# Optimization experiments

Measured on AMD Instinct MI355X. Metric: run time of the kernel, lower is better.

Reference implementation:

```python
import jax, jax.numpy as jnp
import numpy as np

ROPE_THETA = 10000.0


def rope(t, rot_dim):
    """lucidrains-style rotary embedding: rotate first rot_dim features,
    interleaved (x0,x1) pairing; remaining features pass through.
    t: [B, S, D] with rot_dim <= D."""
    S = t.shape[-2]
    half = rot_dim // 2
    inv_freq = 1.0 / (ROPE_THETA ** (jnp.arange(0, rot_dim, 2, dtype=jnp.float32) / rot_dim))  # [half]
    freqs = jnp.arange(S, dtype=jnp.float32)[:, None] * inv_freq[None, :]  # [S, half]
    freqs = jnp.repeat(freqs, 2, axis=-1)  # [S, rot_dim]
    cos, sin = jnp.cos(freqs), jnp.sin(freqs)
    t_rot, t_pass = t[..., :rot_dim], t[..., rot_dim:]
    x = t_rot.reshape(*t_rot.shape[:-1], half, 2)
    rh = jnp.stack([-x[..., 1], x[..., 0]], axis=-1).reshape(t_rot.shape)  # rotate_half (interleaved)
    t_rot = t_rot * cos + rh * sin
    return jnp.concatenate([t_rot, t_pass], axis=-1)


def feature_map(x):
    # L2 normalize along the feature dim (Hydra-attention canonical choice)
    norm = jnp.sqrt(jnp.sum(x * x, axis=-1, keepdims=True))
    return x / jnp.maximum(norm, 1e-12)


def setup_inputs() -> dict:
    key = jax.random.key(0)
    kx, kwi, kwo = jax.random.split(key, 3)
    B, S, D = 8, 4096, 2048
    scale = 0.02  # keep activations numerically tame
    return {
        "X": jax.random.normal(kx, (B, S, D), dtype=jnp.float32),
        "W_in": jax.random.normal(kwi, (3 * D, D), dtype=jnp.float32) * scale,
        "b_in": jnp.zeros((3 * D,), dtype=jnp.float32),
        "W_out": jax.random.normal(kwo, (D, D), dtype=jnp.float32) * scale,
        "b_out": jnp.zeros((D,), dtype=jnp.float32),
    }


def reference(X, W_in, b_in, W_out, b_out):
    D = X.shape[-1]
    QKV = jnp.einsum("bsd,ed->bse", X, W_in) + b_in  # [B, S, 3D]
    Q, K, V = jnp.split(QKV, 3, axis=-1)
    rot_dim = D // 2  # RotaryEmbedding(feature_dim // 2)
    Q = rope(Q, rot_dim)
    K = rope(K, rot_dim)
    A = jnp.sum(feature_map(K) * V, axis=-2)  # [B, D] global sum over sequence
    Y = A[:, None, :] * Q  # [B, S, D]
    Y = jnp.einsum("bsd,ed->bse", Y, W_out) + b_out
    return Y + X
```

## Files before the change

### kernel.cpp

```cpp
#include <hip/hip_runtime.h>

#define N_TOK   32768L
#define DMODEL  2048L
#define E1      6144L
#define ROT     1024
#define SMASK   4095

typedef __attribute__((ext_vector_type(8))) _Float16 half8;
typedef __attribute__((ext_vector_type(4))) _Float16 half4;
typedef __attribute__((ext_vector_type(4))) float    floatx4;
typedef __attribute__((ext_vector_type(4))) float    float4v;

__device__ inline void gld16(const void* g, void* l) {
  __builtin_amdgcn_global_load_lds(
      (const __attribute__((address_space(1))) unsigned int*)g,
      (__attribute__((address_space(3))) unsigned int*)l,
      16, 0, 0);
}

__global__ __launch_bounds__(256) void k_f2h(const float* __restrict__ in,
                                             _Float16* __restrict__ out,
                                             long nElem) {
  long i = ((long)blockIdx.x * 256 + threadIdx.x) * 4;
  if (i + 3 < nElem) {
    float4v v = *(const float4v*)(in + i);
    half4 o;
    o[0] = (_Float16)v[0]; o[1] = (_Float16)v[1];
    o[2] = (_Float16)v[2]; o[3] = (_Float16)v[3];
    *(half4*)(out + i) = o;
  }
}

__global__ __launch_bounds__(256) void k_zero(float* __restrict__ p, int n) {
  int i = blockIdx.x * 256 + threadIdx.x;
  if (i < n) p[i] = 0.f;
}

__global__ __launch_bounds__(256) void k_tab(float2* __restrict__ tab) {
  int i = blockIdx.x * 256 + threadIdx.x;
  int s = i >> 9, j = i & 511;
  float invf = (float)pow(10000.0, -(double)j / 512.0);
  float ang  = (float)s * invf;
  double sd, cd; sincos((double)ang, &sd, &cd);
  float2 o; o.x = (float)cd; o.y = (float)sd;
  tab[i] = o;
}


#define MM(qm, qn) do { \
  _Pragma("unroll") for (int m4 = 0; m4 < 4; m4++) \
  _Pragma("unroll") for (int n2 = 0; n2 < 2; n2++) { \
    acc[(qm)*4+m4][(qn)*2+n2] = __builtin_amdgcn_mfma_f32_16x16x32_f16( \
        af[m4][0], bf[n2][0], acc[(qm)*4+m4][(qn)*2+n2], 0, 0, 0); \
    acc[(qm)*4+m4][(qn)*2+n2] = __builtin_amdgcn_mfma_f32_16x16x32_f16( \
        af[m4][1], bf[n2][1], acc[(qm)*4+m4][(qn)*2+n2], 0, 0, 0); \
  } } while (0)

#define LD_A(buf, qm) do { \
  const _Float16* pA_ = &As[(buf)*16384 + (qm)*8192 + baseA]; \
  _Pragma("unroll") for (int m4 = 0; m4 < 4; m4++) { \
    af[m4][0] = *(const half8*)(pA_ + m4*1024 + okA0); \
    af[m4][1] = *(const half8*)(pA_ + m4*1024 + okA1); \
  } } while (0)

#define LD_B(buf, qn) do { \
  const _Float16* pB_ = &Bs[(buf)*16384 + (qn)*8192 + baseB]; \
  _Pragma("unroll") for (int n2 = 0; n2 < 2; n2++) { \
    bf[n2][0] = *(const half8*)(pB_ + n2*1024 + okB0); \
    bf[n2][1] = *(const half8*)(pB_ + n2*1024 + okB1); \
  } } while (0)

#define STG_A(buf, h, kt) do { \
  const _Float16* gA_ = gA + (long)(h)*128*LDA + (long)(kt)*64; \
  gld16(gA_,          dA + (buf)*16384 + (h)*8192); \
  gld16(gA_ + 8*LDA,  dA + (buf)*16384 + (h)*8192 + 512); \
  } while (0)

#define STG_B(buf, h, kt) do { \
  const _Float16* gB_ = gB + (long)(h)*128*2048 + (long)(kt)*64; \
  gld16(gB_,          dB + (buf)*16384 + (h)*8192); \
  gld16(gB_ + 8*2048, dB + (buf)*16384 + (h)*8192 + 512); \
  } while (0)

#define VM6  asm volatile("s_waitcnt vmcnt(6)" ::: "memory")
#define VM0  asm volatile("s_waitcnt vmcnt(0)" ::: "memory")
#define LG8  asm volatile("s_waitcnt lgkmcnt(8)" ::: "memory")
#define NOP_ ((void)0)

#define PHASE(LDRD, STG, HINT, MMA_, WV) do { \
  LDRD; STG; HINT; \
  asm volatile("" ::: "memory"); \
  __builtin_amdgcn_s_barrier(); \
  asm volatile("s_waitcnt lgkmcnt(0)" ::: "memory"); \
  __builtin_amdgcn_sched_barrier(0); \
  __builtin_amdgcn_s_setprio(1); \
  MMA_; \
  __builtin_amdgcn_s_setprio(0); \
  WV; \
  asm volatile("" ::: "memory"); \
  __builtin_amdgcn_s_barrier(); \
  asm volatile("" ::: "memory"); \
  } while (0)

template <int EB, long LDA, long LDC, bool FP32OUT>
__global__ __launch_bounds__(512, 2) void k_gemm256(
    const _Float16* __restrict__ Ag, const _Float16* __restrict__ Bg,
    const float* __restrict__ bias, const float* __restrict__ Xres,
    void* __restrict__ Cout) {
  __shared__ _Float16 As[32768];
  __shared__ _Float16 Bs[32768];

  const int t    = threadIdx.x;
  const int w    = t >> 6;
  const int l    = t & 63;
  const int quad = l >> 4;
  const int ln   = l & 15;
  const int wr   = w >> 2;
  const int wc   = w & 3;

  const int nwg = 128 * EB;
  const int bid = ((int)blockIdx.x & 7) * (nwg >> 3) + ((int)blockIdx.x >> 3);
  const int eb  = bid % EB;
  const int mb  = bid / EB;
  const long mRow0 = (long)mb * 256;
  const long eCol0 = (long)eb * 256;

  const int stR = (w << 4) + (l >> 3);
  const int stC = ((l & 7) ^ (l >> 3)) << 3;
  const _Float16* gA = Ag + (mRow0 + stR) * LDA  + stC;
  const _Float16* gB = Bg + (eCol0 + stR) * 2048 + stC;
  _Float16* dA = &As[(w * 128 + l) * 8];
  _Float16* dB = &Bs[(w * 128 + l) * 8];

  const int rA = (wr << 6) + ln;
  const int rB = (wc << 5) + ln;
  const int baseA = rA * 64;
  const int baseB = rB * 64;
  const int okA0 = ((quad    ) ^ (rA & 7)) << 3;
  const int okA1 = ((quad ^ 4) ^ (rA & 7)) << 3;
  const int okB0 = ((quad    ) ^ (rB & 7)) << 3;
  const int okB1 = ((quad ^ 4) ^ (rB & 7)) << 3;

  floatx4 acc[8][4];
#pragma unroll
  for (int i = 0; i < 8; i++)
#pragma unroll
    for (int j = 0; j < 4; j++) acc[i][j] = (floatx4){0.f, 0.f, 0.f, 0.f};
  half8 af[4][2], bf[2][2];

  STG_A(0, 0, 0); STG_B(0, 0, 0); STG_B(0, 1, 0); STG_A(0, 1, 0);
  STG_A(1, 0, 1); STG_B(1, 1, 1); STG_A(1, 1, 1);
  VM6;
  asm volatile("" ::: "memory");
  __builtin_amdgcn_s_barrier();
  asm volatile("" ::: "memory");

#pragma unroll 1
  for (int it = 0; it < 15; ++it) {
    const int T = it * 2;
    PHASE({ LD_A(0,0); LD_B(0,0); }, STG_B(1,0,T+1), LG8,  MM(0,0), NOP_);
    PHASE(LD_B(0,1),                 STG_A(0,0,T+2), NOP_, MM(0,1), NOP_);
    PHASE(LD_A(0,1),                 STG_B(0,1,T+2), NOP_, MM(1,1), NOP_);
    PHASE(LD_B(0,0),                 STG_A(0,1,T+2), NOP_, MM(1,0), VM6);
    PHASE({ LD_A(1,0); LD_B(1,0); }, STG_B(0,0,T+2), LG8,  MM(0,0), NOP_);
    PHASE(LD_B(1,1),                 STG_A(1,0,T+3), NOP_, MM(0,1), NOP_);
    PHASE(LD_A(1,1),                 STG_B(1,1,T+3), NOP_, MM(1,1), NOP_);
    PHASE(LD_B(1,0),                 STG_A(1,1,T+3), NOP_, MM(1,0), VM6);
  }
  PHASE({ LD_A(0,0); LD_B(0,0); }, STG_B(1,0,31), LG8,  MM(0,0), NOP_);
  PHASE(LD_B(0,1),                 NOP_,          NOP_, MM(0,1), NOP_);
  PHASE(LD_A(0,1),                 NOP_,          NOP_, MM(1,1), NOP_);
  PHASE(LD_B(0,0),                 NOP_,          NOP_, MM(1,0), VM0);
  PHASE({ LD_A(1,0); LD_B(1,0); }, NOP_,          LG8,  MM(0,0), NOP_);
  PHASE(LD_B(1,1),                 NOP_,          NOP_, MM(0,1), NOP_);
  PHASE(LD_A(1,1),                 NOP_,          NOP_, MM(1,1), NOP_);
  PHASE(LD_B(1,0),                 NOP_,          NOP_, MM(1,0), NOP_);

#pragma unroll
  for (int nt = 0; nt < 4; nt++) {
    const long e = eCol0 + ((nt >> 1) * 128 + (wc << 5) + ((nt & 1) << 4) + ln);
    const float bi = bias[e];
#pragma unroll
    for (int mt = 0; mt < 8; mt++) {
      const long m0 = mRow0 +
          ((mt >> 2) * 128 + (wr << 6) + ((mt & 3) << 4) + (quad << 2));
#pragma unroll
      for (int r = 0; r < 4; r++) {
        const long m = m0 + r;
        if constexpr (FP32OUT) {
          ((float*)Cout)[m * LDC + e] = acc[mt][nt][r] + bi + Xres[m * LDC + e];
        } else {
          ((_Float16*)Cout)[m * LDC + e] = (_Float16)(acc[mt][nt][r] + bi);
        }
      }
    }
  }
}

__global__ __launch_bounds__(256) void k_reduce_a(
    const _Float16* __restrict__ QKV, const float2* __restrict__ tab,
    float* __restrict__ A) {
  const int t  = threadIdx.x;
  const int w  = t >> 6;
  const int l  = t & 63;
  const int wg = blockIdx.x * 4 + w;
  const long row0 = (long)wg * 16;
  const int b  = (int)(row0 >> 12);
  const int d0 = l * 32;

  float acc[32];
  for (int j = 0; j < 32; j++) acc[j] = 0.f;

  for (int i = 0; i < 16; i++) {
    const long n = row0 + i;
    const int  s = (int)(n & SMASK);
    const _Float16* Kr = QKV + n * E1 + DMODEL     + d0;
    const _Float16* Vr = QKV + n * E1 + 2 * DMODEL + d0;
    float kx[32];
    for (int c = 0; c < 4; c++) {
      half8 h = *(const half8*)(Kr + c * 8);
      for (int j = 0; j < 8; j++) kx[c * 8 + j] = (float)h[j];
    }
    if (d0 < ROT) {
      const float2* trow = tab + ((long)s << 9) + (d0 >> 1);
      for (int p = 0; p < 16; p++) {
        float2 cs2 = trow[p];
        float x0 = kx[2 * p], x1 = kx[2 * p + 1];
        kx[2 * p]     = x0 * cs2.x - x1 * cs2.y;
        kx[2 * p + 1] = x1 * cs2.x + x0 * cs2.y;
      }
    }
    float ss = 0.f;
    for (int j = 0; j < 32; j++) ss += kx[j] * kx[j];
    for (int off = 32; off; off >>= 1) ss += __shfl_xor(ss, off);
    const float sc = 1.0f / fmaxf(sqrtf(ss), 1e-12f);
    for (int c = 0; c < 4; c++) {
      half8 h = *(const half8*)(Vr + c * 8);
      for (int j = 0; j < 8; j++)
        acc[c * 8 + j] += kx[c * 8 + j] * sc * (float)h[j];
    }
  }
  float* Ap = A + (long)b * DMODEL + d0;
  for (int j = 0; j < 32; j++) atomicAdd(&Ap[j], acc[j]);
}

__global__ __launch_bounds__(256) void k_make_y1(
    _Float16* __restrict__ QKV, const float2* __restrict__ tab,
    const float* __restrict__ A) {
  const long idx = (long)blockIdx.x * 256 + threadIdx.x;
  const long n   = idx >> 8;
  const int  c   = (int)(idx & 255);
  const int  d   = c * 8;
  const int  b   = (int)(n >> 12);
  const int  s   = (int)(n & SMASK);
  _Float16* Qp = QKV + n * E1 + d;
  half8 h = *(half8*)Qp;
  float x[8];
  for (int j = 0; j < 8; j++) x[j] = (float)h[j];
  if (d < ROT) {
    const float2* trow = tab + ((long)s << 9) + (d >> 1);
    for (int p = 0; p < 4; p++) {
      float2 cs2 = trow[p];
      float x0 = x[2 * p], x1 = x[2 * p + 1];
      x[2 * p]     = x0 * cs2.x - x1 * cs2.y;
      x[2 * p + 1] = x1 * cs2.x + x0 * cs2.y;
    }
  }
  const float* Ap = A + (long)b * DMODEL + d;
  for (int j = 0; j < 8; j++) x[j] *= Ap[j];
  half8 o;
  for (int j = 0; j < 8; j++) o[j] = (_Float16)x[j];
  *(half8*)Qp = o;
}

extern "C" void kernel_launch(void* const* d_in, const int* in_sizes, int n_in,
                              void* d_out, int out_size, void* d_ws, size_t ws_size,
                              hipStream_t stream) {
  const float* X     = (const float*)d_in[0];
  const float* W_in  = (const float*)d_in[1];
  const float* b_in  = (const float*)d_in[2];
  const float* W_out = (const float*)d_in[3];
  const float* b_out = (const float*)d_in[4];
  float* Out = (float*)d_out;

  char* ws = (char*)d_ws;
  _Float16* Xh  = (_Float16*)(ws);
  _Float16* W1h = (_Float16*)(ws + 134217728L);
  _Float16* W2h = (_Float16*)(ws + 159383552L);
  _Float16* QKV = (_Float16*)(ws + 167772160L);
  float*    A   = (float*)  (ws + 570425344L);
  float2*   TAB = (float2*)(ws);

  k_f2h<<<65536, 256, 0, stream>>>(X,     Xh,  N_TOK * DMODEL);
  k_f2h<<<12288, 256, 0, stream>>>(W_in,  W1h, E1 * DMODEL);
  k_f2h<<< 4096, 256, 0, stream>>>(W_out, W2h, DMODEL * DMODEL);
  k_zero<<<64, 256, 0, stream>>>(A, 8 * (int)DMODEL);

  k_gemm256<24, 2048L, 6144L, false><<<3072, 512, 0, stream>>>(
      Xh, W1h, b_in, nullptr, QKV);
  k_tab<<<8192, 256, 0, stream>>>(TAB);
  k_reduce_a<<<512, 256, 0, stream>>>(QKV, TAB, A);
  k_make_y1<<<32768, 256, 0, stream>>>(QKV, TAB, A);
  k_gemm256<8, 6144L, 2048L, true><<<1024, 512, 0, stream>>>(
      QKV, W2h, b_out, X, Out);
}
```

Measured before the change: 1.935 ms.

## Replace atomic K·V reduction with two-stage partial-sum reduction

The sequence reduction for A now writes per-block partial sums, pre-reduced across waves in shared memory, and a second small kernel sums them. This replaces global float atomics and the zeroing kernel. Each block now handles 16 rows split 4 per wave, and the grid grows from 512 to 2048 blocks for more parallelism. The cost is an extra 16 MB partial buffer plus an additional kernel launch, and the summation order becomes deterministic.

```diff
diff --git a/kernel.cpp b/kernel.cpp
--- a/kernel.cpp
+++ b/kernel.cpp
@@ -29,11 +29,6 @@
     o[2] = (_Float16)v[2]; o[3] = (_Float16)v[3];
     *(half4*)(out + i) = o;
   }
-}
-
-__global__ __launch_bounds__(256) void k_zero(float* __restrict__ p, int n) {
-  int i = blockIdx.x * 256 + threadIdx.x;
-  if (i < n) p[i] = 0.f;
 }
 
 __global__ __launch_bounds__(256) void k_tab(float2* __restrict__ tab) {
@@ -197,21 +192,20 @@
   }
 }
 
-__global__ __launch_bounds__(256) void k_reduce_a(
+__global__ __launch_bounds__(256) void k_reduce_part(
     const _Float16* __restrict__ QKV, const float2* __restrict__ tab,
-    float* __restrict__ A) {
+    float* __restrict__ Part) {
+  __shared__ float red[4][32][64];
   const int t  = threadIdx.x;
   const int w  = t >> 6;
   const int l  = t & 63;
-  const int wg = blockIdx.x * 4 + w;
-  const long row0 = (long)wg * 16;
-  const int b  = (int)(row0 >> 12);
+  const long row0 = (long)blockIdx.x * 16 + w * 4;
   const int d0 = l * 32;
 
   float acc[32];
   for (int j = 0; j < 32; j++) acc[j] = 0.f;
 
-  for (int i = 0; i < 16; i++) {
+  for (int i = 0; i < 4; i++) {
     const long n = row0 + i;
     const int  s = (int)(n & SMASK);
     const _Float16* Kr = QKV + n * E1 + DMODEL     + d0;
@@ -240,8 +234,30 @@
         acc[c * 8 + j] += kx[c * 8 + j] * sc * (float)h[j];
     }
   }
-  float* Ap = A + (long)b * DMODEL + d0;
-  for (int j = 0; j < 32; j++) atomicAdd(&Ap[j], acc[j]);
+  for (int j = 0; j < 32; j++) red[w][j][l] = acc[j];
+  __syncthreads();
+  float out[8];
+  for (int j = 0; j < 8; j++) {
+    const int d = t * 8 + j;
+    const int lsrc = d >> 5, jsrc = d & 31;
+    out[j] = red[0][jsrc][lsrc] + red[1][jsrc][lsrc] +
+             red[2][jsrc][lsrc] + red[3][jsrc][lsrc];
+  }
+  float* Pp = Part + (long)blockIdx.x * 2048 + t * 8;
+  *(float4v*)(Pp)     = (float4v){out[0], out[1], out[2], out[3]};
+  *(float4v*)(Pp + 4) = (float4v){out[4], out[5], out[6], out[7]};
+}
+
+__global__ __launch_bounds__(256) void k_reduce_final(
+    const float* __restrict__ Part, float* __restrict__ A) {
+  const int i = blockIdx.x * 256 + threadIdx.x;
+  const int b = i >> 11;
+  const int d = i & 2047;
+  const float* p = Part + (long)b * 256 * 2048 + d;
+  float s = 0.f;
+#pragma unroll 8
+  for (int c = 0; c < 256; c++) s += p[(long)c * 2048];
+  A[i] = s;
 }
 
 __global__ __launch_bounds__(256) void k_make_y1(
@@ -290,16 +306,17 @@
   _Float16* QKV = (_Float16*)(ws + 167772160L);
   float*    A   = (float*)  (ws + 570425344L);
   float2*   TAB = (float2*)(ws);
+  float*    PART= (float*)  (ws + 33554432L);
 
   k_f2h<<<65536, 256, 0, stream>>>(X,     Xh,  N_TOK * DMODEL);
   k_f2h<<<12288, 256, 0, stream>>>(W_in,  W1h, E1 * DMODEL);
   k_f2h<<< 4096, 256, 0, stream>>>(W_out, W2h, DMODEL * DMODEL);
-  k_zero<<<64, 256, 0, stream>>>(A, 8 * (int)DMODEL);
 
   k_gemm256<24, 2048L, 6144L, false><<<3072, 512, 0, stream>>>(
       Xh, W1h, b_in, nullptr, QKV);
   k_tab<<<8192, 256, 0, stream>>>(TAB);
-  k_reduce_a<<<512, 256, 0, stream>>>(QKV, TAB, A);
+  k_reduce_part<<<2048, 256, 0, stream>>>(QKV, TAB, PART);
+  k_reduce_final<<<64, 256, 0, stream>>>(PART, A);
   k_make_y1<<<32768, 256, 0, stream>>>(QKV, TAB, A);
   k_gemm256<8, 6144L, 2048L, true><<<1024, 512, 0, stream>>>(
       QKV, W2h, b_out, X, Out);
```

Result: faster. 1.767 ms (-8.7%).
